# Kernel optimization log

Hardware: AMD Instinct MI355X
Metric: run time of the kernel (lower is better)

The kernel has to match this reference:

```python
import jax, jax.numpy as jnp
import numpy as np
import math

DIM = 147      # input feature dim
EMB = 64       # in_dim * head_cnt
M = 32         # int(EMB * kernel_ratio)
EPS_LN = 1e-5
EPS = 1e-8


def layer_norm(x, g, b, eps=EPS_LN):
    mu = jnp.mean(x, axis=-1, keepdims=True)
    var = jnp.mean(jnp.square(x - mu), axis=-1, keepdims=True)
    return (x - mu) * jax.lax.rsqrt(var + eps) * g + b


def prm_exp(x, W_rf):
    # x: [b, t, e], W_rf: [m, e]
    xd = 0.5 * jnp.sum(x * x, axis=-1, keepdims=True)        # [b, t, 1]
    wtx = jnp.einsum('bte,me->btm', x, W_rf)                  # [b, t, m]
    return jnp.exp(wtx - xd) / math.sqrt(M)


def setup_inputs() -> dict:
    key = jax.random.key(0)
    ks = jax.random.split(key, 16)
    B, T = 32, 3136
    s_in = 1.0 / math.sqrt(DIM)
    s_emb = 1.0 / math.sqrt(EMB)
    inp = {
        'x':      jax.random.normal(ks[0], (B, T, DIM), jnp.float32),
        'w_kqv':  jax.random.uniform(ks[1], (3 * EMB, DIM), jnp.float32, -s_in, s_in),
        'b_kqv':  jax.random.uniform(ks[2], (3 * EMB,), jnp.float32, -s_in, s_in),
        'w_proj': jax.random.uniform(ks[3], (EMB, EMB), jnp.float32, -s_emb, s_emb),
        'b_proj': jax.random.uniform(ks[4], (EMB,), jnp.float32, -s_emb, s_emb),
        'g1':     jnp.ones((DIM,), jnp.float32),
        'beta1':  jnp.zeros((DIM,), jnp.float32),
        'g2':     jnp.ones((EMB,), jnp.float32),
        'beta2':  jnp.zeros((EMB,), jnp.float32),
        'w_m1':   jax.random.uniform(ks[5], (EMB, EMB), jnp.float32, -s_emb, s_emb),
        'b_m1':   jax.random.uniform(ks[6], (EMB,), jnp.float32, -s_emb, s_emb),
        'w_m2':   jax.random.uniform(ks[7], (EMB, EMB), jnp.float32, -s_emb, s_emb),
        'b_m2':   jax.random.uniform(ks[8], (EMB,), jnp.float32, -s_emb, s_emb),
        # orthogonal random-feature matrix scaled by sqrt(m) (buffer 'w')
        'W_rf':   jnp.asarray(np.linalg.qr(np.random.RandomState(0).randn(EMB, EMB))[0][:M] * math.sqrt(M), jnp.float32),
    }
    return inp


def reference(x, w_kqv, b_kqv, w_proj, b_proj, g1, beta1, g2, beta2,
              w_m1, b_m1, w_m2, b_m2, W_rf):
    # --- single_attn(norm1(x)) ---
    xn = layer_norm(x, g1, beta1)
    kqv = xn @ w_kqv.T + b_kqv                                  # [b, t, 3e]
    k, q, v = jnp.split(kqv, 3, axis=-1)
    kp = prm_exp(k, W_rf)                                       # [b, t, m]
    qp = prm_exp(q, W_rf)                                       # [b, t, m]
    D = jnp.einsum('btm,bm->bt', qp, kp.sum(axis=1))[..., None]  # [b, t, 1]
    kptv = jnp.einsum('bte,btm->bem', v, kp)                    # [b, e, m]
    y = jnp.einsum('btm,bem->bte', qp, kptv) / (D + EPS)        # [b, t, e]
    y = v + (y @ w_proj.T + b_proj)                             # residual on v
    # --- y + mlp(norm2(y)) ---
    yn = layer_norm(y, g2, beta2)
    h = jax.nn.gelu(yn @ w_m1.T + b_m1, approximate=False)
    out = y + (h @ w_m2.T + b_m2)
    return out
```

## Files before the change

### kernel.cpp

```cpp
#include <hip/hip_runtime.h>
#include <hip/hip_bf16.h>

#define BB 32
#define TT 3136
#define DD 147
#define EE 64
#define MM 32
#define BT (BB*TT)

typedef __hip_bfloat16 bf16;
typedef __attribute__((ext_vector_type(8))) short s8v;
typedef __attribute__((ext_vector_type(4))) float f4v;

__device__ __forceinline__ float b2f(bf16 v){ return __bfloat162float(v); }
__device__ __forceinline__ bf16 f2b(float v){ return __float2bfloat16(v); }
__device__ __forceinline__ unsigned pack2(float a, float b){
  union { bf16 h[2]; unsigned u; } cv; cv.h[0]=f2b(a); cv.h[1]=f2b(b); return cv.u;
}

template<typename T>
__device__ __forceinline__ float cvt1(T v);
template<> __device__ __forceinline__ float cvt1<float>(float v){ return v; }
template<> __device__ __forceinline__ float cvt1<bf16>(bf16 v){ return __bfloat162float(v); }

__device__ __forceinline__ int bf16flag(const void* g1){
  return (*(const unsigned*)g1 == 0x3F803F80u) ? 1 : 0;
}

template<typename T>
__device__ void cvt_body(int idx,
    const T* wkqv, const T* bkqv, const T* Wrf, const T* wproj, const T* bproj,
    const T* g2, const T* be2, const T* wm1, const T* bm1, const T* wm2,
    const T* bm2, const T* g1, const T* be1,
    bf16* Bprep, bf16* WrfB, bf16* w0B, float* bprojF,
    float* g2F, float* be2F, bf16* w1B, float* bm1F, bf16* w2B,
    float* bm2F, float* c2F)
{
  if (idx < 30720){
    int n = idx/160, k = idx - n*160;
    Bprep[idx] = f2b(k < DD ? cvt1(wkqv[n*DD + k]) * cvt1(g1[k]) : 0.f);
    return;
  }
  idx -= 30720;
  if (idx < 2048){ WrfB[idx] = f2b(cvt1(Wrf[idx])); return; }
  idx -= 2048;
  if (idx < 4608){
    int e = idx/72, c = idx - e*72;
    w0B[idx] = f2b(c < 64 ? cvt1(wproj[e*64 + c]) : 0.f); return;
  }
  idx -= 4608;
  if (idx < 64){ bprojF[idx] = cvt1(bproj[idx]); return; }
  idx -= 64;
  if (idx < 64){ g2F[idx] = cvt1(g2[idx]); return; }
  idx -= 64;
  if (idx < 64){ be2F[idx] = cvt1(be2[idx]); return; }
  idx -= 64;
  if (idx < 4608){
    int e = idx/72, c = idx - e*72;
    w1B[idx] = f2b(c < 64 ? cvt1(wm1[e*64 + c]) : 0.f); return;
  }
  idx -= 4608;
  if (idx < 64){ bm1F[idx] = cvt1(bm1[idx]); return; }
  idx -= 64;
  if (idx < 4608){
    int e = idx/72, c = idx - e*72;
    w2B[idx] = f2b(c < 64 ? cvt1(wm2[e*64 + c]) : 0.f); return;
  }
  idx -= 4608;
  if (idx < 64){ bm2F[idx] = cvt1(bm2[idx]); return; }
  idx -= 64;
  if (idx < 12288){
    int n = idx>>6, ln = idx&63;
    float s = cvt1(wkqv[n*DD + ln])    * cvt1(be1[ln])
            + cvt1(wkqv[n*DD + 64+ln]) * cvt1(be1[64+ln]);
    if (ln < DD-128)
      s = fmaf(cvt1(wkqv[n*DD + 128+ln]), cvt1(be1[128+ln]), s);
    #pragma unroll
    for (int off=32; off; off>>=1) s += __shfl_xor(s, off);
    if (ln == 0) c2F[n] = s + cvt1(bkqv[n]);
    return;
  }
}

__global__ void k_cvt(const void* wkqv, const void* bkqv, const void* Wrf,
    const void* wproj, const void* bproj, const void* g2, const void* be2,
    const void* wm1, const void* bm1, const void* wm2, const void* bm2,
    const void* g1, const void* be1,
    bf16* Bprep, bf16* WrfB, bf16* w0B, float* bprojF,
    float* g2F, float* be2F, bf16* w1B, float* bm1F, bf16* w2B,
    float* bm2F, float* c2F)
{
  int idx = blockIdx.x*256 + threadIdx.x;
  if (bf16flag(g1))
    cvt_body<bf16>(idx, (const bf16*)wkqv, (const bf16*)bkqv, (const bf16*)Wrf,
      (const bf16*)wproj, (const bf16*)bproj, (const bf16*)g2, (const bf16*)be2,
      (const bf16*)wm1, (const bf16*)bm1, (const bf16*)wm2, (const bf16*)bm2,
      (const bf16*)g1, (const bf16*)be1,
      Bprep, WrfB, w0B, bprojF, g2F, be2F, w1B, bm1F, w2B, bm2F, c2F);
  else
    cvt_body<float>(idx, (const float*)wkqv, (const float*)bkqv, (const float*)Wrf,
      (const float*)wproj, (const float*)bproj, (const float*)g2, (const float*)be2,
      (const float*)wm1, (const float*)bm1, (const float*)wm2, (const float*)bm2,
      (const float*)g1, (const float*)be1,
      Bprep, WrfB, w0B, bprojF, g2F, be2F, w1B, bm1F, w2B, bm2F, c2F);
}

__global__ __launch_bounds__(256,6) void k_a2(
    const void* __restrict__ x, const void* __restrict__ g1,
    const bf16* __restrict__ Bprep, const float* __restrict__ c2F,
    const bf16* __restrict__ WrfB,
    bf16* __restrict__ qp, bf16* __restrict__ v,
    float* __restrict__ kptvP, float* __restrict__ ksumP)
{
  __shared__ __align__(16) char smem[21504];
  __shared__ float ksumW[128];
  bf16* vT   = (bf16*)smem;
  bf16* kpT  = (bf16*)(smem + 9216);

  int tid = threadIdx.x;
  size_t t0 = (size_t)blockIdx.x*64;

  int tw = tid>>6, lane = tid&63, quad = lane>>4, r = lane&15;
  int tRow = tw*16 + quad*4;
  char* strip = smem + tw*5376;
  bf16* lin = (bf16*)strip;
  bf16* aS  = (bf16*)strip;
  bf16* kqW = (bf16*)strip;

  if (bf16flag(g1)){
    const uint4* xg = (const uint4*)((const bf16*)x + (t0 + (size_t)tw*16)*DD);
    uint4* xo = (uint4*)lin;
    #pragma unroll
    for (int k=0; k<5; ++k){
      int c = k*64 + lane;
      if (c < 294) xo[c] = xg[c];
    }
  } else {
    const float4* xg = (const float4*)((const float*)x + (t0 + (size_t)tw*16)*DD);
    uint2* xo = (uint2*)lin;
    #pragma unroll
    for (int k=0; k<10; ++k){
      int c = k*64 + lane;
      if (c < 588){
        float4 f = xg[c];
        uint2 u; u.x = pack2(f.x, f.y); u.y = pack2(f.z, f.w);
        xo[c] = u;
      }
    }
  }

  int ti = lane>>2, sl = lane&3;
  const bf16* srow = lin + ti*DD;
  float xv[37];
  float s1 = 0.f, s2 = 0.f;
  #pragma unroll
  for (int j=0; j<37; ++j){
    int e = sl + 4*j;
    float vx = (e < DD) ? b2f(srow[e]) : 0.f;
    xv[j] = vx;
    s1 += vx;
    s2 = fmaf(vx, vx, s2);
  }
  s1 += __shfl_xor(s1,1); s1 += __shfl_xor(s1,2);
  s2 += __shfl_xor(s2,1); s2 += __shfl_xor(s2,2);
  float mu  = s1 * (1.f/147.f);
  float var = s2 * (1.f/147.f) - mu*mu;
  float rn  = rsqrtf(var + 1e-5f);

  bf16* arow = aS + ti*168;
  #pragma unroll
  for (int j=0; j<37; ++j){
    int e = sl + 4*j;
    if (e < DD)       arow[e] = f2b((xv[j]-mu)*rn);
    else if (e == DD) arow[e] = f2b(0.f);
  }
  arow[148+sl] = f2b(0.f); arow[152+sl] = f2b(0.f); arow[156+sl] = f2b(0.f);

  f4v zero = {0.f,0.f,0.f,0.f};

  f4v acc[12];
  #pragma unroll
  for (int nt=0; nt<12; ++nt) acc[nt] = zero;
  const bf16* aBase = aS + r*168 + quad*8;
  const bf16* bBase = &Bprep[r*160 + quad*8];
  #pragma unroll 1
  for (int ks=0; ks<5; ++ks){
    s8v a = *((const s8v*)(aBase + ks*32));
    #pragma unroll
    for (int nt=0; nt<12; ++nt){
      s8v bw = *((const s8v*)(bBase + nt*16*160 + ks*32));
      acc[nt] = __builtin_amdgcn_mfma_f32_16x16x32_bf16(a, bw, acc[nt], 0,0,0);
    }
  }

  float c2v[12];
  #pragma unroll
  for (int nt=0; nt<12; ++nt) c2v[nt] = c2F[nt*16 + r];

  float vv[4][4];
  #pragma unroll
  for (int nt=8; nt<12; ++nt){
    #pragma unroll
    for (int reg=0; reg<4; ++reg){
      vv[nt-8][reg] = acc[nt][reg] + c2v[nt];
      v[(t0 + tRow + reg)*64 + (nt-8)*16 + r] = f2b(vv[nt-8][reg]);
    }
  }

  float kq[8][4];
  #pragma unroll
  for (int nt=0; nt<8; ++nt)
    #pragma unroll
    for (int reg=0; reg<4; ++reg)
      kq[nt][reg] = acc[nt][reg] + c2v[nt];

  #pragma unroll
  for (int nt=0; nt<8; ++nt)
    #pragma unroll
    for (int reg=0; reg<4; ++reg)
      kqW[(quad*4+reg)*136 + nt*16 + r] = f2b(kq[nt][reg]);

  float xdk[4], xdq[4];
  #pragma unroll
  for (int reg=0; reg<4; ++reg){
    float sk = 0.f, sq = 0.f;
    #pragma unroll
    for (int nt=0; nt<4; ++nt){
      sk = fmaf(kq[nt][reg],   kq[nt][reg],   sk);
      sq = fmaf(kq[nt+4][reg], kq[nt+4][reg], sq);
    }
    #pragma unroll
    for (int off=1; off<16; off<<=1){
      sk += __shfl_xor(sk, off);
      sq += __shfl_xor(sq, off);
    }
    xdk[reg] = 0.5f*sk;
    xdq[reg] = 0.5f*sq;
  }

  f4v accP[2] = {zero, zero}, accQ[2] = {zero, zero};
  #pragma unroll
  for (int ks=0; ks<2; ++ks){
    s8v ak = *((const s8v*)&kqW[r*136 + ks*32 + quad*8]);
    s8v aq = *((const s8v*)&kqW[r*136 + 64 + ks*32 + quad*8]);
    #pragma unroll
    for (int nt=0; nt<2; ++nt){
      s8v wf = *((const s8v*)&WrfB[(nt*16+r)*64 + ks*32 + quad*8]);
      accP[nt] = __builtin_amdgcn_mfma_f32_16x16x32_bf16(ak, wf, accP[nt], 0,0,0);
      accQ[nt] = __builtin_amdgcn_mfma_f32_16x16x32_bf16(aq, wf, accQ[nt], 0,0,0);
    }
  }
  float kpv[2][4];
  #pragma unroll
  for (int nt=0; nt<2; ++nt){
    #pragma unroll
    for (int reg=0; reg<4; ++reg){
      size_t gt = t0 + tRow + reg;
      kpv[nt][reg] = expf(accP[nt][reg] - xdk[reg]) * 0.17677669529663687f;
      qp[gt*32 + nt*16 + r] = f2b(expf(accQ[nt][reg] - xdq[reg]) * 0.17677669529663687f);
    }
  }
  __syncthreads();

  #pragma unroll
  for (int nt=0; nt<4; ++nt){
    *((unsigned*)&vT[(nt*16+r)*72 + tRow])     = pack2(vv[nt][0], vv[nt][1]);
    *((unsigned*)&vT[(nt*16+r)*72 + tRow + 2]) = pack2(vv[nt][2], vv[nt][3]);
  }
  #pragma unroll
  for (int nt=0; nt<2; ++nt){
    *((unsigned*)&kpT[(nt*16+r)*72 + tRow])     = pack2(kpv[nt][0], kpv[nt][1]);
    *((unsigned*)&kpT[(nt*16+r)*72 + tRow + 2]) = pack2(kpv[nt][2], kpv[nt][3]);
  }

  float ks0 = kpv[0][0]+kpv[0][1]+kpv[0][2]+kpv[0][3];
  float ks1 = kpv[1][0]+kpv[1][1]+kpv[1][2]+kpv[1][3];
  ks0 += __shfl_xor(ks0, 16); ks0 += __shfl_xor(ks0, 32);
  ks1 += __shfl_xor(ks1, 16); ks1 += __shfl_xor(ks1, 32);
  if (lane < 16){
    ksumW[tw*32 + r]      = ks0;
    ksumW[tw*32 + 16 + r] = ks1;
  }
  __syncthreads();

  if (tid < 32)
    ksumP[(size_t)blockIdx.x*32 + tid] =
      ksumW[tid] + ksumW[32+tid] + ksumW[64+tid] + ksumW[96+tid];

  f4v accKV[2] = {zero, zero};
  #pragma unroll
  for (int kh=0; kh<2; ++kh){
    s8v av = *((const s8v*)&vT[(tw*16+r)*72 + kh*32 + quad*8]);
    #pragma unroll
    for (int nt=0; nt<2; ++nt){
      s8v bk = *((const s8v*)&kpT[(nt*16+r)*72 + kh*32 + quad*8]);
      accKV[nt] = __builtin_amdgcn_mfma_f32_16x16x32_bf16(av, bk, accKV[nt], 0,0,0);
    }
  }
  float* dst = kptvP + (size_t)blockIdx.x*2048;
  #pragma unroll
  for (int nt=0; nt<2; ++nt)
    #pragma unroll
    for (int reg=0; reg<4; ++reg)
      dst[(tw*16 + quad*4 + reg)*32 + nt*16 + r] = accKV[nt][reg];
}

__global__ void k_red(const float* __restrict__ kptvP,
                      const float* __restrict__ ksumP,
                      float* __restrict__ kptvF, float* __restrict__ ksumF){
  int idx = blockIdx.x*256 + threadIdx.x;
  if (idx < 65536){
    int b = idx >> 11, i = idx & 2047;
    const float* src = kptvP + (size_t)b*49*2048 + i;
    float s = 0.f;
    #pragma unroll 7
    for (int j=0; j<49; ++j) s += src[j*2048];
    kptvF[idx] = s;
  } else if (idx < 66560){
    int k = idx - 65536;
    int b = k >> 5, m = k & 31;
    const float* src = ksumP + (size_t)b*49*32 + m;
    float s = 0.f;
    #pragma unroll 7
    for (int j=0; j<49; ++j) s += src[j*32];
    ksumF[k] = s;
  }
}

__global__ __launch_bounds__(256,5) void k_b(
    const bf16* __restrict__ qp, const bf16* __restrict__ v,
    const float* __restrict__ kptvF, const float* __restrict__ ksumF,
    const bf16* __restrict__ w0B, const float* __restrict__ bprojF,
    const float* __restrict__ g2F, const float* __restrict__ be2F,
    const bf16* __restrict__ w1B, const float* __restrict__ bm1F,
    const bf16* __restrict__ w2B, const float* __restrict__ bm2F,
    const void* __restrict__ g1, void* __restrict__ outp)
{
  __shared__ __align__(16) bf16 qpS[64*40];
  __shared__ __align__(16) bf16 kvS[64*40];
  __shared__ __align__(16) bf16 vS[64*72];
  __shared__ __align__(16) bf16 stA[64*72];
  __shared__ float ksS[32];
  __shared__ float bpS[64], b1S[64], b2S[64], gS[64], btS[64];

  int flag = bf16flag(g1);
  int tid = threadIdx.x;
  int b = blockIdx.y;
  int gt0 = b*TT + blockIdx.x*64;

  {
    int t = tid>>2, q = tid&3;
    uint4 u = ((const uint4*)(qp + (size_t)gt0*32))[tid];
    *((uint4*)&qpS[t*40 + q*8]) = u;
  }
  for (int i=tid; i<512; i+=256){
    int e = i>>3, q = i&7;
    float4 f = ((const float4*)(kptvF + b*2048))[i];
    union { bf16 h[4]; uint2 u; } cv;
    cv.h[0]=f2b(f.x); cv.h[1]=f2b(f.y); cv.h[2]=f2b(f.z); cv.h[3]=f2b(f.w);
    *((uint2*)&kvS[e*40 + q*4]) = cv.u;
  }
  for (int i=tid; i<512; i+=256){
    int t = i>>3, q = i&7;
    uint4 u = ((const uint4*)(v + (size_t)gt0*64))[i];
    *((uint4*)&vS[t*72 + q*8]) = u;
  }
  if (tid<32) ksS[tid] = ksumF[b*32+tid];
  if (tid<64){
    bpS[tid]=bprojF[tid]; b1S[tid]=bm1F[tid]; b2S[tid]=bm2F[tid];
    gS[tid]=g2F[tid]; btS[tid]=be2F[tid];
  }
  __syncthreads();

  int tw = tid>>6, lane = tid&63, quad = lane>>4, r = lane&15;
  int tRow = tw*16 + quad*4;
  f4v zero = {0.f,0.f,0.f,0.f};

  float dpart;
  {
    int ti = lane>>2, sl = lane&3;
    const bf16* qrow = &qpS[(tw*16+ti)*40];
    float s = 0.f;
    #pragma unroll
    for (int m=0; m<8; ++m) s = fmaf(b2f(qrow[sl*8+m]), ksS[sl*8+m], s);
    s += __shfl_xor(s,1); s += __shfl_xor(s,2);
    dpart = s;
  }
  float Dinv[4];
  #pragma unroll
  for (int reg=0; reg<4; ++reg){
    float d = __shfl(dpart, (lane & 0x30) + 4*reg);
    Dinv[reg] = 1.f/(d + 1e-8f);
  }

  f4v accA[4];
  {
    s8v aq = *((const s8v*)&qpS[(tw*16+r)*40 + quad*8]);
    #pragma unroll
    for (int nt=0; nt<4; ++nt){
      s8v bk = *((const s8v*)&kvS[(nt*16+r)*40 + quad*8]);
      accA[nt] = __builtin_amdgcn_mfma_f32_16x16x32_bf16(aq, bk, zero, 0,0,0);
    }
  }

  #pragma unroll
  for (int nt=0; nt<4; ++nt)
    #pragma unroll
    for (int reg=0; reg<4; ++reg)
      stA[(tRow+reg)*72 + nt*16 + r] = f2b(accA[nt][reg]*Dinv[reg]);

  f4v accY[4] = {zero, zero, zero, zero};
  #pragma unroll
  for (int kh=0; kh<2; ++kh){
    s8v ay = *((const s8v*)&stA[(tw*16+r)*72 + kh*32 + quad*8]);
    #pragma unroll
    for (int nt=0; nt<4; ++nt){
      s8v bw = *((const s8v*)&w0B[(nt*16+r)*72 + kh*32 + quad*8]);
      accY[nt] = __builtin_amdgcn_mfma_f32_16x16x32_bf16(ay, bw, accY[nt], 0,0,0);
    }
  }
  float y[4][4];
  #pragma unroll
  for (int nt=0; nt<4; ++nt){
    int e = nt*16 + r;
    float bp = bpS[e];
    #pragma unroll
    for (int reg=0; reg<4; ++reg)
      y[nt][reg] = accY[nt][reg] + b2f(vS[(tRow+reg)*72 + e]) + bp;
  }

  float mu[4], rs[4];
  #pragma unroll
  for (int reg=0; reg<4; ++reg){
    float s = y[0][reg]+y[1][reg]+y[2][reg]+y[3][reg];
    #pragma unroll
    for (int off=1; off<16; off<<=1) s += __shfl_xor(s, off);
    mu[reg] = s * (1.f/64.f);
  }
  #pragma unroll
  for (int reg=0; reg<4; ++reg){
    float d2 = 0.f;
    #pragma unroll
    for (int nt=0; nt<4; ++nt){ float d = y[nt][reg]-mu[reg]; d2 = fmaf(d,d,d2); }
    #pragma unroll
    for (int off=1; off<16; off<<=1) d2 += __shfl_xor(d2, off);
    rs[reg] = rsqrtf(d2*(1.f/64.f) + 1e-5f);
  }
  #pragma unroll
  for (int nt=0; nt<4; ++nt){
    int e = nt*16 + r;
    float g = gS[e], be = btS[e];
    #pragma unroll
    for (int reg=0; reg<4; ++reg)
      stA[(tRow+reg)*72 + e] = f2b((y[nt][reg]-mu[reg])*rs[reg]*g + be);
  }

  f4v accH[4] = {zero, zero, zero, zero};
  #pragma unroll
  for (int kh=0; kh<2; ++kh){
    s8v ah = *((const s8v*)&stA[(tw*16+r)*72 + kh*32 + quad*8]);
    #pragma unroll
    for (int nt=0; nt<4; ++nt){
      s8v bw = *((const s8v*)&w1B[(nt*16+r)*72 + kh*32 + quad*8]);
      accH[nt] = __builtin_amdgcn_mfma_f32_16x16x32_bf16(ah, bw, accH[nt], 0,0,0);
    }
  }
  #pragma unroll
  for (int nt=0; nt<4; ++nt){
    int e = nt*16 + r;
    float b1 = b1S[e];
    #pragma unroll
    for (int reg=0; reg<4; ++reg){
      float h = accH[nt][reg] + b1;
      h = 0.5f*h*(1.f + erff(h*0.70710678118654752f));
      stA[(tRow+reg)*72 + e] = f2b(h);
    }
  }

  f4v accO[4] = {zero, zero, zero, zero};
  #pragma unroll
  for (int kh=0; kh<2; ++kh){
    s8v ao = *((const s8v*)&stA[(tw*16+r)*72 + kh*32 + quad*8]);
    #pragma unroll
    for (int nt=0; nt<4; ++nt){
      s8v bw = *((const s8v*)&w2B[(nt*16+r)*72 + kh*32 + quad*8]);
      accO[nt] = __builtin_amdgcn_mfma_f32_16x16x32_bf16(ao, bw, accO[nt], 0,0,0);
    }
  }
  if (flag){
    bf16* o = (bf16*)outp;
    #pragma unroll
    for (int nt=0; nt<4; ++nt){
      int e = nt*16 + r;
      float b2 = b2S[e];
      #pragma unroll
      for (int reg=0; reg<4; ++reg)
        o[(size_t)(gt0 + tRow + reg)*64 + e] = f2b(y[nt][reg] + accO[nt][reg] + b2);
    }
  } else {
    float* o = (float*)outp;
    #pragma unroll
    for (int nt=0; nt<4; ++nt){
      int e = nt*16 + r;
      float b2 = b2S[e];
      #pragma unroll
      for (int reg=0; reg<4; ++reg)
        o[(size_t)(gt0 + tRow + reg)*64 + e] = y[nt][reg] + accO[nt][reg] + b2;
    }
  }
}

extern "C" void kernel_launch(void* const* d_in, const int* in_sizes, int n_in,
                              void* d_out, int out_size, void* d_ws, size_t ws_size,
                              hipStream_t stream){
  const void* x    = d_in[0];
  const void* wkqv = d_in[1];
  const void* bkqv = d_in[2];
  const void* wproj= d_in[3];
  const void* bproj= d_in[4];
  const void* g1   = d_in[5];
  const void* be1  = d_in[6];
  const void* g2   = d_in[7];
  const void* be2  = d_in[8];
  const void* wm1  = d_in[9];
  const void* bm1  = d_in[10];
  const void* wm2  = d_in[11];
  const void* bm2  = d_in[12];
  const void* Wrf  = d_in[13];

  char* ws = (char*)d_ws;
  bf16*  Bprep = (bf16*) (ws + 256);
  bf16*  WrfB  = (bf16*) (ws + 62464);
  bf16*  w0B   = (bf16*) (ws + 66560);
  float* bprojF= (float*)(ws + 82944);
  float* g2F   = (float*)(ws + 83200);
  float* be2F  = (float*)(ws + 83456);
  bf16*  w1B   = (bf16*) (ws + 83712);
  float* bm1F  = (float*)(ws + 100096);
  bf16*  w2B   = (bf16*) (ws + 100352);
  float* bm2F  = (float*)(ws + 116736);
  float* c2F   = (float*)(ws + 118784);
  float* kptvP = (float*)(ws + 131072);
  float* ksumP = (float*)(ws + 12976128);
  float* kptvF = (float*)(ws + 32231424);
  float* ksumF = (float*)(ws + 32493568);
  bf16*  qp    = (bf16*) (ws + 32497664);
  bf16*  v     = (bf16*) (ws + 38920192);

  k_cvt<<<256, 256, 0, stream>>>(wkqv, bkqv, Wrf, wproj, bproj, g2, be2,
      wm1, bm1, wm2, bm2, g1, be1,
      Bprep, WrfB, w0B, bprojF, g2F, be2F, w1B, bm1F, w2B, bm2F, c2F);
  k_a2<<<BT/64, 256, 0, stream>>>(x, g1, Bprep, c2F, WrfB,
      qp, v, kptvP, ksumP);
  k_red<<<260, 256, 0, stream>>>(kptvP, ksumP, kptvF, ksumF);
  k_b<<<dim3(TT/64, BB), 256, 0, stream>>>(qp, v, kptvF, ksumF,
      w0B, bprojF, g2F, be2F, w1B, bm1F, w2B, bm2F, g1, d_out);
}
```

Before: 193.6 us.

## Stage qp and v through LDS for coalesced 16-byte stores and transposed intermediate layout

k_a2 now writes qp and v into shared-memory transposed tiles and copies them to global as contiguous uint4 rows per block, replacing scattered 2-byte global stores. k_b reads the new per-block transposed layout, scattering qp into LDS and indexing v transposed, and stages the bf16 output through LDS so it can be written with vectorized stores. Launch bounds for k_a2 drop from 6 to 4 waves per SIMD, giving more registers but potentially lowering occupancy, and the extra LDS traffic and syncs add some cost.

```diff
diff --git a/kernel.cpp b/kernel.cpp
--- a/kernel.cpp
+++ b/kernel.cpp
@@ -105,17 +105,18 @@
       Bprep, WrfB, w0B, bprojF, g2F, be2F, w1B, bm1F, w2B, bm2F, c2F);
 }
 
-__global__ __launch_bounds__(256,6) void k_a2(
+__global__ __launch_bounds__(256,4) void k_a2(
     const void* __restrict__ x, const void* __restrict__ g1,
     const bf16* __restrict__ Bprep, const float* __restrict__ c2F,
     const bf16* __restrict__ WrfB,
-    bf16* __restrict__ qp, bf16* __restrict__ v,
+    bf16* __restrict__ qpG, bf16* __restrict__ vG,
     float* __restrict__ kptvP, float* __restrict__ ksumP)
 {
   __shared__ __align__(16) char smem[21504];
   __shared__ float ksumW[128];
   bf16* vT   = (bf16*)smem;
   bf16* kpT  = (bf16*)(smem + 9216);
+  bf16* qpT  = (bf16*)(smem + 13824);
 
   int tid = threadIdx.x;
   size_t t0 = (size_t)blockIdx.x*64;
@@ -199,13 +200,10 @@
 
   float vv[4][4];
   #pragma unroll
-  for (int nt=8; nt<12; ++nt){
-    #pragma unroll
-    for (int reg=0; reg<4; ++reg){
+  for (int nt=8; nt<12; ++nt)
+    #pragma unroll
+    for (int reg=0; reg<4; ++reg)
       vv[nt-8][reg] = acc[nt][reg] + c2v[nt];
-      v[(t0 + tRow + reg)*64 + (nt-8)*16 + r] = f2b(vv[nt-8][reg]);
-    }
-  }
 
   float kq[8][4];
   #pragma unroll
@@ -250,14 +248,13 @@
       accQ[nt] = __builtin_amdgcn_mfma_f32_16x16x32_bf16(aq, wf, accQ[nt], 0,0,0);
     }
   }
-  float kpv[2][4];
+  float kpv[2][4], qpv[2][4];
   #pragma unroll
   for (int nt=0; nt<2; ++nt){
     #pragma unroll
     for (int reg=0; reg<4; ++reg){
-      size_t gt = t0 + tRow + reg;
       kpv[nt][reg] = expf(accP[nt][reg] - xdk[reg]) * 0.17677669529663687f;
-      qp[gt*32 + nt*16 + r] = f2b(expf(accQ[nt][reg] - xdq[reg]) * 0.17677669529663687f);
+      qpv[nt][reg] = expf(accQ[nt][reg] - xdq[reg]) * 0.17677669529663687f;
     }
   }
   __syncthreads();
@@ -271,6 +268,8 @@
   for (int nt=0; nt<2; ++nt){
     *((unsigned*)&kpT[(nt*16+r)*72 + tRow])     = pack2(kpv[nt][0], kpv[nt][1]);
     *((unsigned*)&kpT[(nt*16+r)*72 + tRow + 2]) = pack2(kpv[nt][2], kpv[nt][3]);
+    *((unsigned*)&qpT[(nt*16+r)*72 + tRow])     = pack2(qpv[nt][0], qpv[nt][1]);
+    *((unsigned*)&qpT[(nt*16+r)*72 + tRow + 2]) = pack2(qpv[nt][2], qpv[nt][3]);
   }
 
   float ks0 = kpv[0][0]+kpv[0][1]+kpv[0][2]+kpv[0][3];
@@ -283,6 +282,18 @@
   }
   __syncthreads();
 
+  {
+    uint4* vg = (uint4*)(vG + (size_t)blockIdx.x*4096);
+    for (int i=tid; i<512; i+=256){
+      int e = i>>3, q = i&7;
+      vg[i] = *((const uint4*)&vT[e*72 + q*8]);
+    }
+    uint4* qg = (uint4*)(qpG + (size_t)blockIdx.x*2048);
+    {
+      int m = tid>>3, q = tid&7;
+      qg[tid] = *((const uint4*)&qpT[m*72 + q*8]);
+    }
+  }
   if (tid < 32)
     ksumP[(size_t)blockIdx.x*32 + tid] =
       ksumW[tid] + ksumW[32+tid] + ksumW[64+tid] + ksumW[96+tid];
@@ -328,7 +339,7 @@
 }
 
 __global__ __launch_bounds__(256,5) void k_b(
-    const bf16* __restrict__ qp, const bf16* __restrict__ v,
+    const bf16* __restrict__ qpG, const bf16* __restrict__ vG,
     const float* __restrict__ kptvF, const float* __restrict__ ksumF,
     const bf16* __restrict__ w0B, const float* __restrict__ bprojF,
     const float* __restrict__ g2F, const float* __restrict__ be2F,
@@ -347,11 +358,15 @@
   int tid = threadIdx.x;
   int b = blockIdx.y;
   int gt0 = b*TT + blockIdx.x*64;
+  int blk = b*49 + blockIdx.x;
 
   {
-    int t = tid>>2, q = tid&3;
-    uint4 u = ((const uint4*)(qp + (size_t)gt0*32))[tid];
-    *((uint4*)&qpS[t*40 + q*8]) = u;
+    int m = tid>>3, q = tid&7;
+    union { uint4 u4; bf16 h[8]; } cv;
+    cv.u4 = ((const uint4*)(qpG + (size_t)blk*2048))[tid];
+    #pragma unroll
+    for (int j=0; j<8; ++j)
+      qpS[(q*8+j)*40 + m] = cv.h[j];
   }
   for (int i=tid; i<512; i+=256){
     int e = i>>3, q = i&7;
@@ -361,9 +376,8 @@
     *((uint2*)&kvS[e*40 + q*4]) = cv.u;
   }
   for (int i=tid; i<512; i+=256){
-    int t = i>>3, q = i&7;
-    uint4 u = ((const uint4*)(v + (size_t)gt0*64))[i];
-    *((uint4*)&vS[t*72 + q*8]) = u;
+    int e = i>>3, q = i&7;
+    *((uint4*)&vS[e*72 + q*8]) = ((const uint4*)(vG + (size_t)blk*4096))[i];
   }
   if (tid<32) ksS[tid] = ksumF[b*32+tid];
   if (tid<64){
@@ -426,7 +440,7 @@
     float bp = bpS[e];
     #pragma unroll
     for (int reg=0; reg<4; ++reg)
-      y[nt][reg] = accY[nt][reg] + b2f(vS[(tRow+reg)*72 + e]) + bp;
+      y[nt][reg] = accY[nt][reg] + b2f(vS[e*72 + (tRow+reg)]) + bp;
   }
 
   float mu[4], rs[4];
@@ -488,14 +502,19 @@
     }
   }
   if (flag){
-    bf16* o = (bf16*)outp;
     #pragma unroll
     for (int nt=0; nt<4; ++nt){
       int e = nt*16 + r;
       float b2 = b2S[e];
       #pragma unroll
       for (int reg=0; reg<4; ++reg)
-        o[(size_t)(gt0 + tRow + reg)*64 + e] = f2b(y[nt][reg] + accO[nt][reg] + b2);
+        stA[(tRow+reg)*72 + e] = f2b(y[nt][reg] + accO[nt][reg] + b2);
+    }
+    __syncthreads();
+    bf16* o = (bf16*)outp + (size_t)gt0*64;
+    for (int i=tid; i<512; i+=256){
+      int t = i>>3, q = i&7;
+      *((uint4*)(o + t*64 + q*8)) = *((const uint4*)&stA[t*72 + q*8]);
     }
   } else {
     float* o = (float*)outp;
@@ -544,15 +563,15 @@
   float* ksumP = (float*)(ws + 12976128);
   float* kptvF = (float*)(ws + 32231424);
   float* ksumF = (float*)(ws + 32493568);
-  bf16*  qp    = (bf16*) (ws + 32497664);
-  bf16*  v     = (bf16*) (ws + 38920192);
+  bf16*  qpG   = (bf16*) (ws + 32497664);
+  bf16*  vG    = (bf16*) (ws + 38920192);
 
   k_cvt<<<256, 256, 0, stream>>>(wkqv, bkqv, Wrf, wproj, bproj, g2, be2,
       wm1, bm1, wm2, bm2, g1, be1,
       Bprep, WrfB, w0B, bprojF, g2F, be2F, w1B, bm1F, w2B, bm2F, c2F);
   k_a2<<<BT/64, 256, 0, stream>>>(x, g1, Bprep, c2F, WrfB,
-      qp, v, kptvP, ksumP);
+      qpG, vG, kptvP, ksumP);
   k_red<<<260, 256, 0, stream>>>(kptvP, ksumP, kptvF, ksumF);
-  k_b<<<dim3(TT/64, BB), 256, 0, stream>>>(qp, v, kptvF, ksumF,
+  k_b<<<dim3(TT/64, BB), 256, 0, stream>>>(qpG, vG, kptvF, ksumF,
       w0B, bprojF, g2F, be2F, w1B, bm1F, w2B, bm2F, g1, d_out);
 }
```

New measurement: 180.5 us. 1.07x faster.
